# Kernel tuning notes

Hardware: AMD Instinct MI355X
Metric: run time of the kernel (lower is better)

## Reference

```python
import jax, jax.numpy as jnp
import numpy as np

N_ATOM = 2_000_000
N_FRAG = 200_000
EPS = 1e-4


def setup_inputs() -> dict:
    key = jax.random.key(0)
    k1, k2, k3, k4, k5 = jax.random.split(key, 5)
    f_atom = jax.random.normal(k1, (N_ATOM, 3), dtype=jnp.float32)
    atom_pos = jax.random.normal(k2, (N_ATOM, 3), dtype=jnp.float32) * 5.0
    T_frag = jax.random.normal(k3, (N_FRAG, 3), dtype=jnp.float32) * 5.0
    frag_id = jax.random.randint(k4, (N_ATOM,), 0, N_FRAG, dtype=jnp.int32)
    frag_sizes = jax.random.randint(k5, (N_FRAG,), 0, 30, dtype=jnp.int32)
    return {
        "f_atom": f_atom,
        "atom_pos": atom_pos,
        "T_frag": T_frag,
        "frag_id": frag_id,
        "n_frag": N_FRAG,
        "frag_sizes": frag_sizes,
    }


def reference(f_atom, atom_pos, T_frag, frag_id, n_frag, frag_sizes):
    """Newton-Euler aggregation: per-atom forces -> fragment (v, omega)."""
    seg = lambda x: jax.ops.segment_sum(x, frag_id, num_segments=n_frag)

    # scatter_mean of forces -> translational velocity [n_frag, 3]
    counts = seg(jnp.ones((f_atom.shape[0],), dtype=f_atom.dtype))  # [n_frag]
    v_frag = seg(f_atom) / jnp.maximum(counts, 1.0)[:, None]

    # lever arms and torques
    r_arm = atom_pos - T_frag[frag_id]                 # [N_atom, 3]
    torque = seg(jnp.cross(r_arm, f_atom))            # [n_frag, 3]

    # inertia tensor: I = sum(r^2) * eye - sum(r r^T)  (+ eps regularization)
    r2 = jnp.sum(r_arm * r_arm, axis=-1)              # [N_atom]
    I_diag = seg(r2)                                   # [n_frag]
    I_off = seg(r_arm[:, :, None] * r_arm[:, None, :])  # [n_frag, 3, 3]
    eye3 = jnp.eye(3, dtype=f_atom.dtype)
    I_tensor = I_diag[:, None, None] * eye3 - I_off + EPS * eye3

    # batched 3x3 solve for angular velocity
    omega_frag = jnp.linalg.solve(I_tensor, torque[..., None])[..., 0]

    # zero omega for single-atom fragments
    single_mask = (frag_sizes <= 1)[:, None]
    omega_frag = jnp.where(single_mask, jnp.zeros_like(omega_frag), omega_frag)
    return v_frag, omega_frag
```

## Files before the change

### kernel.cpp

```cpp
#include <hip/hip_runtime.h>


#define BSHIFT 9
#define BFRAGS (1 << BSHIFT)
#define NBMAX  512
#define NACC   13

#define B_THREADS 1024
#define TILE_B    2048
#define NT_B      2
#define CHUNK     (TILE_B * 2)
#define R_THREADS 512
#define TILE      1024

__global__ void atom_accum_kernel(const float* __restrict__ f_atom,
                                  const float* __restrict__ atom_pos,
                                  const float* __restrict__ T_frag,
                                  const int*   __restrict__ frag_id,
                                  float* __restrict__ acc,
                                  int n_atom, int n_frag) {
    int i = blockIdx.x * blockDim.x + threadIdx.x;
    if (i >= n_atom) return;
    float fx = f_atom[3 * i + 0], fy = f_atom[3 * i + 1], fz = f_atom[3 * i + 2];
    float px = atom_pos[3 * i + 0], py = atom_pos[3 * i + 1], pz = atom_pos[3 * i + 2];
    int fid = frag_id[i];
    float rx = px - T_frag[3 * fid + 0];
    float ry = py - T_frag[3 * fid + 1];
    float rz = pz - T_frag[3 * fid + 2];
    atomicAdd(&acc[0 * n_frag + fid], 1.0f);
    atomicAdd(&acc[1 * n_frag + fid], fx);
    atomicAdd(&acc[2 * n_frag + fid], fy);
    atomicAdd(&acc[3 * n_frag + fid], fz);
    atomicAdd(&acc[4 * n_frag + fid], ry * fz - rz * fy);
    atomicAdd(&acc[5 * n_frag + fid], rz * fx - rx * fz);
    atomicAdd(&acc[6 * n_frag + fid], rx * fy - ry * fx);
    atomicAdd(&acc[7 * n_frag + fid], rx * rx);
    atomicAdd(&acc[8 * n_frag + fid], ry * ry);
    atomicAdd(&acc[9 * n_frag + fid], rz * rz);
    atomicAdd(&acc[10 * n_frag + fid], rx * ry);
    atomicAdd(&acc[11 * n_frag + fid], rx * rz);
    atomicAdd(&acc[12 * n_frag + fid], ry * rz);
}

__device__ __forceinline__ void solve_frag(const float s[NACC], int fs,
                                           float* vout, float* oout) {
    float inv_cnt = 1.0f / fmaxf(s[0], 1.0f);
    vout[0] = s[1] * inv_cnt;
    vout[1] = s[2] * inv_cnt;
    vout[2] = s[3] * inv_cnt;

    double sxx = (double)s[7], syy = (double)s[8], szz = (double)s[9];
    double sxy = (double)s[10], sxz = (double)s[11], syz = (double)s[12];
    const double eps = 1e-4;
    double d = sxx + syy + szz;
    double a00 = d - sxx + eps, a11 = d - syy + eps, a22 = d - szz + eps;
    double a01 = -sxy, a02 = -sxz, a12 = -syz;

    double c00 = a11 * a22 - a12 * a12;
    double c01 = a02 * a12 - a01 * a22;
    double c02 = a01 * a12 - a02 * a11;
    double det = a00 * c00 + a01 * c01 + a02 * c02;
    double inv_det = (det != 0.0) ? 1.0 / det : 0.0;
    double c11 = a00 * a22 - a02 * a02;
    double c12 = a01 * a02 - a00 * a12;
    double c22 = a00 * a11 - a01 * a01;

    double tx = (double)s[4], ty = (double)s[5], tz = (double)s[6];
    if (fs <= 1) {
        oout[0] = 0.0f; oout[1] = 0.0f; oout[2] = 0.0f;
    } else {
        oout[0] = (float)((c00 * tx + c01 * ty + c02 * tz) * inv_det);
        oout[1] = (float)((c01 * tx + c11 * ty + c12 * tz) * inv_det);
        oout[2] = (float)((c02 * tx + c12 * ty + c22 * tz) * inv_det);
    }
}

__global__ void finalize_accum_kernel(const float* __restrict__ acc,
                                      const int* __restrict__ frag_sizes,
                                      float* __restrict__ out, int n_frag) {
    int i = blockIdx.x * blockDim.x + threadIdx.x;
    if (i >= n_frag) return;
    float s[NACC];
#pragma unroll
    for (int c = 0; c < NACC; ++c) s[c] = acc[(size_t)c * n_frag + i];
    float v[3], o[3];
    solve_frag(s, frag_sizes[i], v, o);
    out[3 * i + 0] = v[0]; out[3 * i + 1] = v[1]; out[3 * i + 2] = v[2];
    float* om = out + 3 * (size_t)n_frag;
    om[3 * i + 0] = o[0]; om[3 * i + 1] = o[1]; om[3 * i + 2] = o[2];
}


__device__ __forceinline__ int xcd_swizzle(int orig, int n) {
    int q = n >> 3, r = n & 7;
    int xcd = orig & 7, slot = orig >> 3;
    return (xcd < r ? xcd * (q + 1) : r * (q + 1) + (xcd - r) * q) + slot;
}

__global__ __launch_bounds__(B_THREADS)
void hist_kernel(const int* __restrict__ frag_id, unsigned* __restrict__ h,
                 int n_atom, int nb) {
    __shared__ unsigned hh[NBMAX];
    int tid = threadIdx.x;
    if (tid < NBMAX) hh[tid] = 0;
    __syncthreads();
    int c0 = blockIdx.x * CHUNK;
    int cend = min(c0 + CHUNK, n_atom);
    for (int i = c0 + tid; i < cend; i += B_THREADS)
        atomicAdd(&hh[frag_id[i] >> BSHIFT], 1u);
    __syncthreads();
    size_t row = (size_t)blockIdx.x * nb;
    if (tid < nb) h[row + tid] = hh[tid];
}

__global__ void colscan_kernel(unsigned* __restrict__ h, unsigned* __restrict__ T,
                               int nb, int nreg) {
    int wid = (blockIdx.x * blockDim.x + threadIdx.x) >> 6;
    int lane = threadIdx.x & 63;
    if (wid >= nb) return;
    unsigned run = 0;
    for (int k0 = 0; k0 < nreg; k0 += 64) {
        int k = k0 + lane;
        unsigned v = (k < nreg) ? h[(size_t)k * nb + wid] : 0u;
        unsigned incl = v;
#pragma unroll
        for (int o = 1; o < 64; o <<= 1) {
            unsigned x = __shfl_up(incl, o);
            if (lane >= o) incl += x;
        }
        if (k < nreg) h[(size_t)k * nb + wid] = run + (incl - v);
        run += __shfl(incl, 63);
    }
    if (lane == 0) T[wid] = run;
}

__global__ __launch_bounds__(1024)
void gscan_kernel(const unsigned* __restrict__ T, unsigned* __restrict__ gstart,
                  int nb) {
    __shared__ unsigned s[1024];
    int t = threadIdx.x;
    unsigned v = (t < nb) ? T[t] : 0u;
    s[t] = v;
    __syncthreads();
    for (int o = 1; o < 1024; o <<= 1) {
        unsigned x = (t >= o) ? s[t - o] : 0u;
        __syncthreads();
        s[t] += x;
        __syncthreads();
    }
    if (t < nb) gstart[t] = s[t] - v;
    if (t == 0) gstart[nb] = s[nb - 1];
}

__global__ __launch_bounds__(B_THREADS)
void build_kernel(const float* __restrict__ f_atom,
                  const float* __restrict__ atom_pos,
                  const float* __restrict__ T_frag,
                  const int* __restrict__ frag_id,
                  const unsigned* __restrict__ h,
                  const unsigned* __restrict__ gstart,
                  float* __restrict__ payload,
                  int n_atom, int nb, int nreg) {
    __shared__ float stage[TILE_B * 8];
    __shared__ unsigned cursor[NBMAX];
    __shared__ unsigned cnt[NBMAX];
    __shared__ unsigned tfs[NBMAX];
    __shared__ unsigned wsum[B_THREADS / 64];

    int tid = threadIdx.x;
    int wave = tid >> 6, lane = tid & 63;
    int blk = xcd_swizzle(blockIdx.x, nreg);

    size_t row = (size_t)blk * nb;
    if (tid < nb) cursor[tid] = gstart[tid] + h[row + tid];

    int c0 = blk * CHUNK;
    int cend = min(c0 + CHUNK, n_atom);

    for (int tbase = c0; tbase < cend; tbase += TILE_B) {
        int tcount = min(TILE_B, cend - tbase);
        if (tid < NBMAX) cnt[tid] = 0;
        __syncthreads();

        float4 p0j[NT_B], p1j[NT_B];
        unsigned rankj[NT_B]; int bj[NT_B]; bool actj[NT_B];
#pragma unroll
        for (int j = 0; j < NT_B; ++j) {
            int i = tbase + tid + j * B_THREADS;
            actj[j] = (i < cend);
            bj[j] = 0; rankj[j] = 0;
            if (actj[j]) {
                int fid = frag_id[i];
                int b = fid >> BSHIFT;
                bj[j] = b;
                rankj[j] = atomicAdd(&cnt[b], 1u);
                float fx = f_atom[3 * i + 0], fy = f_atom[3 * i + 1],
                      fz = f_atom[3 * i + 2];
                float rx = atom_pos[3 * i + 0] - T_frag[3 * fid + 0];
                float ry = atom_pos[3 * i + 1] - T_frag[3 * fid + 1];
                float rz = atom_pos[3 * i + 2] - T_frag[3 * fid + 2];
                unsigned dst = cursor[b] + rankj[j];
                p0j[j] = make_float4(fx, fy, fz, __int_as_float(fid));
                p1j[j] = make_float4(rx, ry, rz, __uint_as_float(dst));
            }
        }
        __syncthreads();

        unsigned v = (tid < NBMAX) ? cnt[tid] : 0u;
        unsigned incl = v;
#pragma unroll
        for (int o = 1; o < 64; o <<= 1) {
            unsigned x = __shfl_up(incl, o);
            if (lane >= o) incl += x;
        }
        if (lane == 63) wsum[wave] = incl;
        __syncthreads();
        unsigned wbase = 0;
#pragma unroll
        for (int w = 0; w < B_THREADS / 64; ++w)
            wbase += (w < wave) ? wsum[w] : 0u;
        if (tid < NBMAX) tfs[tid] = wbase + incl - v;
        __syncthreads();

#pragma unroll
        for (int j = 0; j < NT_B; ++j) {
            if (actj[j]) {
                unsigned slot = tfs[bj[j]] + rankj[j];
                float4* d = (float4*)&stage[(size_t)slot * 8];
                d[0] = p0j[j];
                d[1] = p1j[j];
            }
        }
        __syncthreads();

        for (int s = tid; s < tcount; s += B_THREADS) {
            const float4* q = (const float4*)&stage[(size_t)s * 8];
            float4 a = q[0];
            float4 c = q[1];
            unsigned dst = __float_as_uint(c.w);
            float4* p = (float4*)(payload + (size_t)dst * 8);
            p[0] = a;
            p[1] = c;
        }
        if (tid < nb) cursor[tid] += cnt[tid];
    }
}

__global__ __launch_bounds__(R_THREADS)
void reduce_kernel(const float* __restrict__ payload,
                   const unsigned* __restrict__ gstart,
                   const int* __restrict__ frag_sizes,
                   float* __restrict__ out, int n_frag, int nb) {
    __shared__ float stage[TILE * 8];
    __shared__ unsigned cnt[BFRAGS];
    __shared__ unsigned fstart[BFRAGS + 1];
    __shared__ unsigned wsum[R_THREADS / 64];

    int b = xcd_swizzle(blockIdx.x, nb);
    int tid = threadIdx.x;
    int wave = tid >> 6, lane = tid & 63;
    unsigned s0 = gstart[b], s1 = gstart[b + 1];

    float m0 = 0.f, m1 = 0.f, m2 = 0.f, m3 = 0.f, m4 = 0.f, m5 = 0.f,
          m6 = 0.f, m7 = 0.f, m8 = 0.f, m9 = 0.f, m10 = 0.f, m11 = 0.f,
          m12 = 0.f;

    for (unsigned tbase = s0; tbase < s1; tbase += TILE) {
        cnt[tid] = 0;
        __syncthreads();

        float4 p0j[2], p1j[2];
        unsigned rankj[2]; int lfj[2]; bool actj[2];
#pragma unroll
        for (int j = 0; j < 2; ++j) {
            unsigned s = tbase + (unsigned)tid + (unsigned)j * R_THREADS;
            actj[j] = (s < s1);
            lfj[j] = 0; rankj[j] = 0;
            if (actj[j]) {
                const float4* p = (const float4*)(payload + (size_t)s * 8);
                p0j[j] = p[0];
                p1j[j] = p[1];
                lfj[j] = __float_as_int(p0j[j].w) & (BFRAGS - 1);
                rankj[j] = atomicAdd(&cnt[lfj[j]], 1u);
            }
        }
        __syncthreads();

        unsigned v = cnt[tid];
        unsigned incl = v;
#pragma unroll
        for (int o = 1; o < 64; o <<= 1) {
            unsigned x = __shfl_up(incl, o);
            if (lane >= o) incl += x;
        }
        if (lane == 63) wsum[wave] = incl;
        __syncthreads();
        unsigned wbase = 0;
#pragma unroll
        for (int w = 0; w < R_THREADS / 64; ++w)
            wbase += (w < wave) ? wsum[w] : 0u;
        fstart[tid] = wbase + incl - v;
        if (tid == R_THREADS - 1) fstart[BFRAGS] = wbase + incl;
        __syncthreads();

#pragma unroll
        for (int j = 0; j < 2; ++j) {
            if (actj[j]) {
                unsigned slot = fstart[lfj[j]] + rankj[j];
                float4* d = (float4*)&stage[(size_t)slot * 8];
                d[0] = p0j[j];
                d[1] = p1j[j];
            }
        }
        __syncthreads();

        unsigned e0 = fstart[tid], e1 = fstart[tid + 1];
        for (unsigned u = e0; u < e1; ++u) {
            const float4* q = (const float4*)&stage[(size_t)u * 8];
            float4 a = q[0];
            float4 c = q[1];
            float fx = a.x, fy = a.y, fz = a.z;
            float rx = c.x, ry = c.y, rz = c.z;
            m0 += 1.0f;
            m1 += fx; m2 += fy; m3 += fz;
            m4 += ry * fz - rz * fy;
            m5 += rz * fx - rx * fz;
            m6 += rx * fy - ry * fx;
            m7 += rx * rx; m8 += ry * ry; m9 += rz * rz;
            m10 += rx * ry; m11 += rx * rz; m12 += ry * rz;
        }
        __syncthreads();
    }

    int fid = (b << BSHIFT) + tid;
    if (fid < n_frag) {
        float sv[NACC] = {m0, m1, m2, m3, m4, m5, m6,
                          m7, m8, m9, m10, m11, m12};
        float v[3], o[3];
        solve_frag(sv, frag_sizes[fid], v, o);
        out[3 * fid + 0] = v[0];
        out[3 * fid + 1] = v[1];
        out[3 * fid + 2] = v[2];
        float* om = out + 3 * (size_t)n_frag;
        om[3 * fid + 0] = o[0];
        om[3 * fid + 1] = o[1];
        om[3 * fid + 2] = o[2];
    }
}


static inline size_t pad256(size_t x) { return (x + 255) & ~(size_t)255; }

extern "C" void kernel_launch(void* const* d_in, const int* in_sizes, int n_in,
                              void* d_out, int out_size, void* d_ws, size_t ws_size,
                              hipStream_t stream) {
    const float* f_atom   = (const float*)d_in[0];
    const float* atom_pos = (const float*)d_in[1];
    const float* T_frag   = (const float*)d_in[2];
    const int*   frag_id  = (const int*)d_in[3];
    const int*   frag_sizes = (const int*)d_in[5];

    int n_atom = in_sizes[0] / 3;
    int n_frag = in_sizes[2] / 3;
    int nb   = (n_frag + BFRAGS - 1) >> BSHIFT;
    int nreg = (n_atom + CHUNK - 1) / CHUNK;

    size_t h_bytes   = pad256((size_t)nreg * nb * sizeof(unsigned));
    size_t ctl_bytes = pad256(((size_t)nb + (size_t)nb + 1) * sizeof(unsigned));
    size_t payload_bytes = (size_t)n_atom * 8 * sizeof(float);
    bool sorted_ok = (nb <= NBMAX) &&
                     (h_bytes + ctl_bytes + payload_bytes <= ws_size);

    if (sorted_ok) {
        unsigned* h      = (unsigned*)d_ws;
        unsigned* T      = (unsigned*)((char*)d_ws + h_bytes);
        unsigned* gstart = T + nb;
        float* payload   = (float*)((char*)d_ws + h_bytes + ctl_bytes);

        hist_kernel<<<nreg, B_THREADS, 0, stream>>>(frag_id, h, n_atom, nb);
        int cs_blocks = (nb * 64 + 255) / 256;
        colscan_kernel<<<cs_blocks, 256, 0, stream>>>(h, T, nb, nreg);
        gscan_kernel<<<1, 1024, 0, stream>>>(T, gstart, nb);
        build_kernel<<<nreg, B_THREADS, 0, stream>>>(f_atom, atom_pos, T_frag,
                                                     frag_id, h, gstart, payload,
                                                     n_atom, nb, nreg);
        reduce_kernel<<<nb, R_THREADS, 0, stream>>>(payload, gstart, frag_sizes,
                                                    (float*)d_out, n_frag, nb);
    } else {
        float* acc = (float*)d_ws;
        hipMemsetAsync(acc, 0, (size_t)NACC * n_frag * sizeof(float), stream);
        int threads = 256;
        atom_accum_kernel<<<(n_atom + threads - 1) / threads, threads, 0, stream>>>(
            f_atom, atom_pos, T_frag, frag_id, acc, n_atom, n_frag);
        finalize_accum_kernel<<<(n_frag + threads - 1) / threads, threads, 0, stream>>>(
            acc, frag_sizes, (float*)d_out, n_frag);
    }
}
```

Measured before the change: 87.72 us.

## Replace global histogram/scan pipeline with per-tile local sort and tile-offset lookup

Drops the hist, column-scan and global-scan kernels. Each build block now bucket-sorts its own 2048-atom tile in shared memory, writes it contiguously, and records per-bucket offsets. The reduce kernel scans those per-tile offsets for its bucket and fetches its atoms from every tile using a binary search over the cumulative counts. This removes three launches and the extra pass over frag_id. In exchange, reduce reads become scattered small segments spread across about a thousand tiles, and the XCD swizzle is removed.

```diff
diff --git a/kernel.cpp b/kernel.cpp
--- a/kernel.cpp
+++ b/kernel.cpp
@@ -9,9 +9,10 @@
 #define B_THREADS 1024
 #define TILE_B    2048
 #define NT_B      2
-#define CHUNK     (TILE_B * 2)
 #define R_THREADS 512
 #define TILE      1024
+#define NT_R      2
+#define MAXTILES  1024
 
 __global__ void atom_accum_kernel(const float* __restrict__ f_atom,
                                   const float* __restrict__ atom_pos,
@@ -91,193 +92,167 @@
 }
 
 
-__device__ __forceinline__ int xcd_swizzle(int orig, int n) {
-    int q = n >> 3, r = n & 7;
-    int xcd = orig & 7, slot = orig >> 3;
-    return (xcd < r ? xcd * (q + 1) : r * (q + 1) + (xcd - r) * q) + slot;
-}
-
-__global__ __launch_bounds__(B_THREADS)
-void hist_kernel(const int* __restrict__ frag_id, unsigned* __restrict__ h,
-                 int n_atom, int nb) {
-    __shared__ unsigned hh[NBMAX];
-    int tid = threadIdx.x;
-    if (tid < NBMAX) hh[tid] = 0;
-    __syncthreads();
-    int c0 = blockIdx.x * CHUNK;
-    int cend = min(c0 + CHUNK, n_atom);
-    for (int i = c0 + tid; i < cend; i += B_THREADS)
-        atomicAdd(&hh[frag_id[i] >> BSHIFT], 1u);
-    __syncthreads();
-    size_t row = (size_t)blockIdx.x * nb;
-    if (tid < nb) h[row + tid] = hh[tid];
-}
-
-__global__ void colscan_kernel(unsigned* __restrict__ h, unsigned* __restrict__ T,
-                               int nb, int nreg) {
-    int wid = (blockIdx.x * blockDim.x + threadIdx.x) >> 6;
-    int lane = threadIdx.x & 63;
-    if (wid >= nb) return;
-    unsigned run = 0;
-    for (int k0 = 0; k0 < nreg; k0 += 64) {
-        int k = k0 + lane;
-        unsigned v = (k < nreg) ? h[(size_t)k * nb + wid] : 0u;
-        unsigned incl = v;
-#pragma unroll
-        for (int o = 1; o < 64; o <<= 1) {
-            unsigned x = __shfl_up(incl, o);
-            if (lane >= o) incl += x;
-        }
-        if (k < nreg) h[(size_t)k * nb + wid] = run + (incl - v);
-        run += __shfl(incl, 63);
-    }
-    if (lane == 0) T[wid] = run;
-}
-
-__global__ __launch_bounds__(1024)
-void gscan_kernel(const unsigned* __restrict__ T, unsigned* __restrict__ gstart,
-                  int nb) {
-    __shared__ unsigned s[1024];
-    int t = threadIdx.x;
-    unsigned v = (t < nb) ? T[t] : 0u;
-    s[t] = v;
-    __syncthreads();
-    for (int o = 1; o < 1024; o <<= 1) {
-        unsigned x = (t >= o) ? s[t - o] : 0u;
-        __syncthreads();
-        s[t] += x;
-        __syncthreads();
-    }
-    if (t < nb) gstart[t] = s[t] - v;
-    if (t == 0) gstart[nb] = s[nb - 1];
-}
-
 __global__ __launch_bounds__(B_THREADS)
 void build_kernel(const float* __restrict__ f_atom,
                   const float* __restrict__ atom_pos,
                   const float* __restrict__ T_frag,
                   const int* __restrict__ frag_id,
-                  const unsigned* __restrict__ h,
-                  const unsigned* __restrict__ gstart,
+                  unsigned* __restrict__ off,
                   float* __restrict__ payload,
-                  int n_atom, int nb, int nreg) {
+                  int n_atom, int nb) {
     __shared__ float stage[TILE_B * 8];
-    __shared__ unsigned cursor[NBMAX];
     __shared__ unsigned cnt[NBMAX];
     __shared__ unsigned tfs[NBMAX];
     __shared__ unsigned wsum[B_THREADS / 64];
 
     int tid = threadIdx.x;
     int wave = tid >> 6, lane = tid & 63;
-    int blk = xcd_swizzle(blockIdx.x, nreg);
-
-    size_t row = (size_t)blk * nb;
-    if (tid < nb) cursor[tid] = gstart[tid] + h[row + tid];
-
-    int c0 = blk * CHUNK;
-    int cend = min(c0 + CHUNK, n_atom);
-
-    for (int tbase = c0; tbase < cend; tbase += TILE_B) {
-        int tcount = min(TILE_B, cend - tbase);
-        if (tid < NBMAX) cnt[tid] = 0;
-        __syncthreads();
-
-        float4 p0j[NT_B], p1j[NT_B];
-        unsigned rankj[NT_B]; int bj[NT_B]; bool actj[NT_B];
-#pragma unroll
-        for (int j = 0; j < NT_B; ++j) {
-            int i = tbase + tid + j * B_THREADS;
-            actj[j] = (i < cend);
-            bj[j] = 0; rankj[j] = 0;
-            if (actj[j]) {
-                int fid = frag_id[i];
-                int b = fid >> BSHIFT;
-                bj[j] = b;
-                rankj[j] = atomicAdd(&cnt[b], 1u);
-                float fx = f_atom[3 * i + 0], fy = f_atom[3 * i + 1],
-                      fz = f_atom[3 * i + 2];
-                float rx = atom_pos[3 * i + 0] - T_frag[3 * fid + 0];
-                float ry = atom_pos[3 * i + 1] - T_frag[3 * fid + 1];
-                float rz = atom_pos[3 * i + 2] - T_frag[3 * fid + 2];
-                unsigned dst = cursor[b] + rankj[j];
-                p0j[j] = make_float4(fx, fy, fz, __int_as_float(fid));
-                p1j[j] = make_float4(rx, ry, rz, __uint_as_float(dst));
-            }
-        }
-        __syncthreads();
-
-        unsigned v = (tid < NBMAX) ? cnt[tid] : 0u;
-        unsigned incl = v;
-#pragma unroll
-        for (int o = 1; o < 64; o <<= 1) {
-            unsigned x = __shfl_up(incl, o);
-            if (lane >= o) incl += x;
-        }
-        if (lane == 63) wsum[wave] = incl;
-        __syncthreads();
-        unsigned wbase = 0;
-#pragma unroll
-        for (int w = 0; w < B_THREADS / 64; ++w)
-            wbase += (w < wave) ? wsum[w] : 0u;
-        if (tid < NBMAX) tfs[tid] = wbase + incl - v;
-        __syncthreads();
-
-#pragma unroll
-        for (int j = 0; j < NT_B; ++j) {
-            if (actj[j]) {
-                unsigned slot = tfs[bj[j]] + rankj[j];
-                float4* d = (float4*)&stage[(size_t)slot * 8];
-                d[0] = p0j[j];
-                d[1] = p1j[j];
-            }
-        }
-        __syncthreads();
-
-        for (int s = tid; s < tcount; s += B_THREADS) {
-            const float4* q = (const float4*)&stage[(size_t)s * 8];
-            float4 a = q[0];
-            float4 c = q[1];
-            unsigned dst = __float_as_uint(c.w);
-            float4* p = (float4*)(payload + (size_t)dst * 8);
-            p[0] = a;
-            p[1] = c;
-        }
-        if (tid < nb) cursor[tid] += cnt[tid];
+    int blk = blockIdx.x;
+    int c0 = blk * TILE_B;
+    int cend = min(c0 + TILE_B, n_atom);
+    int tcount = cend - c0;
+
+    if (tid < NBMAX) cnt[tid] = 0;
+    __syncthreads();
+
+    float4 p0j[NT_B], p1j[NT_B];
+    unsigned rankj[NT_B]; int bj[NT_B]; bool actj[NT_B];
+#pragma unroll
+    for (int j = 0; j < NT_B; ++j) {
+        int i = c0 + tid + j * B_THREADS;
+        actj[j] = (i < cend);
+        bj[j] = 0; rankj[j] = 0;
+        if (actj[j]) {
+            int fid = frag_id[i];
+            int b = fid >> BSHIFT;
+            bj[j] = b;
+            rankj[j] = atomicAdd(&cnt[b], 1u);
+            float fx = f_atom[3 * i + 0], fy = f_atom[3 * i + 1],
+                  fz = f_atom[3 * i + 2];
+            float rx = atom_pos[3 * i + 0] - T_frag[3 * fid + 0];
+            float ry = atom_pos[3 * i + 1] - T_frag[3 * fid + 1];
+            float rz = atom_pos[3 * i + 2] - T_frag[3 * fid + 2];
+            p0j[j] = make_float4(fx, fy, fz, __int_as_float(fid));
+            p1j[j] = make_float4(rx, ry, rz, 0.0f);
+        }
+    }
+    __syncthreads();
+
+    unsigned v = (tid < NBMAX) ? cnt[tid] : 0u;
+    unsigned incl = v;
+#pragma unroll
+    for (int o = 1; o < 64; o <<= 1) {
+        unsigned x = __shfl_up(incl, o);
+        if (lane >= o) incl += x;
+    }
+    if (lane == 63) wsum[wave] = incl;
+    __syncthreads();
+    unsigned wbase = 0;
+#pragma unroll
+    for (int w = 0; w < B_THREADS / 64; ++w)
+        wbase += (w < wave) ? wsum[w] : 0u;
+    unsigned excl = wbase + incl - v;
+    if (tid < NBMAX) tfs[tid] = excl;
+
+    size_t row = (size_t)blk * (nb + 1);
+    if (tid < nb) off[row + tid] = excl;
+    if (tid == B_THREADS - 1) off[row + nb] = wbase + incl;
+    __syncthreads();
+
+#pragma unroll
+    for (int j = 0; j < NT_B; ++j) {
+        if (actj[j]) {
+            unsigned slot = tfs[bj[j]] + rankj[j];
+            float4* d = (float4*)&stage[(size_t)slot * 8];
+            d[0] = p0j[j];
+            d[1] = p1j[j];
+        }
+    }
+    __syncthreads();
+
+    for (int s = tid; s < tcount; s += B_THREADS) {
+        const float4* q = (const float4*)&stage[(size_t)s * 8];
+        float4* p = (float4*)(payload + ((size_t)c0 + s) * 8);
+        p[0] = q[0];
+        p[1] = q[1];
     }
 }
 
 __global__ __launch_bounds__(R_THREADS)
 void reduce_kernel(const float* __restrict__ payload,
-                   const unsigned* __restrict__ gstart,
+                   const unsigned* __restrict__ off,
                    const int* __restrict__ frag_sizes,
-                   float* __restrict__ out, int n_frag, int nb) {
+                   float* __restrict__ out,
+                   int n_frag, int nb, int ntiles) {
     __shared__ float stage[TILE * 8];
+    __shared__ unsigned o0s[MAXTILES];
+    __shared__ unsigned cum[MAXTILES + 1];
     __shared__ unsigned cnt[BFRAGS];
     __shared__ unsigned fstart[BFRAGS + 1];
     __shared__ unsigned wsum[R_THREADS / 64];
 
-    int b = xcd_swizzle(blockIdx.x, nb);
+    int b = blockIdx.x;
     int tid = threadIdx.x;
     int wave = tid >> 6, lane = tid & 63;
-    unsigned s0 = gstart[b], s1 = gstart[b + 1];
+    int W = nb + 1;
+
+    int k0 = 2 * tid, k1 = 2 * tid + 1;
+    unsigned l0 = 0, l1 = 0;
+    if (k0 < ntiles) {
+        size_t r = (size_t)k0 * W;
+        unsigned a = off[r + b];
+        o0s[k0] = a;
+        l0 = off[r + b + 1] - a;
+    }
+    if (k1 < ntiles) {
+        size_t r = (size_t)k1 * W;
+        unsigned a = off[r + b];
+        o0s[k1] = a;
+        l1 = off[r + b + 1] - a;
+    }
+    unsigned pr = l0 + l1;
+    unsigned incl = pr;
+#pragma unroll
+    for (int o = 1; o < 64; o <<= 1) {
+        unsigned x = __shfl_up(incl, o);
+        if (lane >= o) incl += x;
+    }
+    if (lane == 63) wsum[wave] = incl;
+    __syncthreads();
+    unsigned wbase = 0;
+#pragma unroll
+    for (int w = 0; w < R_THREADS / 64; ++w)
+        wbase += (w < wave) ? wsum[w] : 0u;
+    unsigned X = wbase + incl - pr;
+    if (k0 < ntiles) cum[k0] = X;
+    if (k1 < ntiles) cum[k1] = X + l0;
+    if (tid == R_THREADS - 1) cum[ntiles] = wbase + incl;
+    __syncthreads();
+    unsigned T = cum[ntiles];
 
     float m0 = 0.f, m1 = 0.f, m2 = 0.f, m3 = 0.f, m4 = 0.f, m5 = 0.f,
           m6 = 0.f, m7 = 0.f, m8 = 0.f, m9 = 0.f, m10 = 0.f, m11 = 0.f,
           m12 = 0.f;
 
-    for (unsigned tbase = s0; tbase < s1; tbase += TILE) {
+    for (unsigned tbase = 0; tbase < T; tbase += TILE) {
         cnt[tid] = 0;
         __syncthreads();
 
-        float4 p0j[2], p1j[2];
-        unsigned rankj[2]; int lfj[2]; bool actj[2];
-#pragma unroll
-        for (int j = 0; j < 2; ++j) {
-            unsigned s = tbase + (unsigned)tid + (unsigned)j * R_THREADS;
-            actj[j] = (s < s1);
+        float4 p0j[NT_R], p1j[NT_R];
+        unsigned rankj[NT_R]; int lfj[NT_R]; bool actj[NT_R];
+#pragma unroll
+        for (int j = 0; j < NT_R; ++j) {
+            unsigned g = tbase + (unsigned)tid + (unsigned)j * R_THREADS;
+            actj[j] = (g < T);
             lfj[j] = 0; rankj[j] = 0;
             if (actj[j]) {
-                const float4* p = (const float4*)(payload + (size_t)s * 8);
+                int lo = 0, hi = ntiles - 1;
+                while (lo < hi) {
+                    int mid = (lo + hi + 1) >> 1;
+                    if (cum[mid] <= g) lo = mid; else hi = mid - 1;
+                }
+                size_t idx = (size_t)lo * TILE_B + o0s[lo] + (g - cum[lo]);
+                const float4* p = (const float4*)(payload + idx * 8);
                 p0j[j] = p[0];
                 p1j[j] = p[1];
                 lfj[j] = __float_as_int(p0j[j].w) & (BFRAGS - 1);
@@ -287,24 +262,24 @@
         __syncthreads();
 
         unsigned v = cnt[tid];
-        unsigned incl = v;
+        unsigned incl2 = v;
 #pragma unroll
         for (int o = 1; o < 64; o <<= 1) {
-            unsigned x = __shfl_up(incl, o);
-            if (lane >= o) incl += x;
-        }
-        if (lane == 63) wsum[wave] = incl;
-        __syncthreads();
-        unsigned wbase = 0;
+            unsigned x = __shfl_up(incl2, o);
+            if (lane >= o) incl2 += x;
+        }
+        if (lane == 63) wsum[wave] = incl2;
+        __syncthreads();
+        unsigned wb2 = 0;
 #pragma unroll
         for (int w = 0; w < R_THREADS / 64; ++w)
-            wbase += (w < wave) ? wsum[w] : 0u;
-        fstart[tid] = wbase + incl - v;
-        if (tid == R_THREADS - 1) fstart[BFRAGS] = wbase + incl;
-        __syncthreads();
-
-#pragma unroll
-        for (int j = 0; j < 2; ++j) {
+            wb2 += (w < wave) ? wsum[w] : 0u;
+        fstart[tid] = wb2 + incl2 - v;
+        if (tid == R_THREADS - 1) fstart[BFRAGS] = wb2 + incl2;
+        __syncthreads();
+
+#pragma unroll
+        for (int j = 0; j < NT_R; ++j) {
             if (actj[j]) {
                 unsigned slot = fstart[lfj[j]] + rankj[j];
                 float4* d = (float4*)&stage[(size_t)slot * 8];
@@ -362,30 +337,22 @@
 
     int n_atom = in_sizes[0] / 3;
     int n_frag = in_sizes[2] / 3;
-    int nb   = (n_frag + BFRAGS - 1) >> BSHIFT;
-    int nreg = (n_atom + CHUNK - 1) / CHUNK;
-
-    size_t h_bytes   = pad256((size_t)nreg * nb * sizeof(unsigned));
-    size_t ctl_bytes = pad256(((size_t)nb + (size_t)nb + 1) * sizeof(unsigned));
-    size_t payload_bytes = (size_t)n_atom * 8 * sizeof(float);
-    bool sorted_ok = (nb <= NBMAX) &&
-                     (h_bytes + ctl_bytes + payload_bytes <= ws_size);
+    int nb     = (n_frag + BFRAGS - 1) >> BSHIFT;
+    int ntiles = (n_atom + TILE_B - 1) / TILE_B;
+
+    size_t off_bytes = pad256((size_t)ntiles * (nb + 1) * sizeof(unsigned));
+    size_t payload_bytes = (size_t)ntiles * TILE_B * 8 * sizeof(float);
+    bool sorted_ok = (nb <= NBMAX) && (ntiles <= MAXTILES) &&
+                     (off_bytes + payload_bytes <= ws_size);
 
     if (sorted_ok) {
-        unsigned* h      = (unsigned*)d_ws;
-        unsigned* T      = (unsigned*)((char*)d_ws + h_bytes);
-        unsigned* gstart = T + nb;
-        float* payload   = (float*)((char*)d_ws + h_bytes + ctl_bytes);
-
-        hist_kernel<<<nreg, B_THREADS, 0, stream>>>(frag_id, h, n_atom, nb);
-        int cs_blocks = (nb * 64 + 255) / 256;
-        colscan_kernel<<<cs_blocks, 256, 0, stream>>>(h, T, nb, nreg);
-        gscan_kernel<<<1, 1024, 0, stream>>>(T, gstart, nb);
-        build_kernel<<<nreg, B_THREADS, 0, stream>>>(f_atom, atom_pos, T_frag,
-                                                     frag_id, h, gstart, payload,
-                                                     n_atom, nb, nreg);
-        reduce_kernel<<<nb, R_THREADS, 0, stream>>>(payload, gstart, frag_sizes,
-                                                    (float*)d_out, n_frag, nb);
+        unsigned* off  = (unsigned*)d_ws;
+        float* payload = (float*)((char*)d_ws + off_bytes);
+
+        build_kernel<<<ntiles, B_THREADS, 0, stream>>>(
+            f_atom, atom_pos, T_frag, frag_id, off, payload, n_atom, nb);
+        reduce_kernel<<<nb, R_THREADS, 0, stream>>>(
+            payload, off, frag_sizes, (float*)d_out, n_frag, nb, ntiles);
     } else {
         float* acc = (float*)d_ws;
         hipMemsetAsync(acc, 0, (size_t)NACC * n_frag * sizeof(float), stream);
```

After: 103.0 us. +17.4%, slower.
